# Optimization experiments

Hardware: AMD Instinct MI355X
Metric: run time of the kernel (lower is better)

The kernel has to match this reference:

```python
import jax, jax.numpy as jnp
import numpy as np

GROUP_SIZE = 64
IN_F, OUT_F, RANK = 4096, 4096, 32
N_TOKENS = 4096
N_GROUPS = IN_F // GROUP_SIZE


def setup_inputs() -> dict:
    key = jax.random.key(0)
    k = jax.random.split(key, 6)
    x = jax.random.normal(k[0], (N_TOKENS, IN_F), dtype=jnp.float32)
    # signed int4 values in [-8, 7], stored unpacked as int32
    main_qweight = jax.random.randint(k[1], (OUT_F, N_GROUPS, GROUP_SIZE), -8, 8, dtype=jnp.int32)
    main_wscale = jax.random.uniform(k[2], (OUT_F, N_GROUPS), dtype=jnp.float32) * 0.02 + 1e-3
    bias = jax.random.normal(k[3], (OUT_F,), dtype=jnp.float32) * 0.02
    proj_down_dense = jax.random.normal(k[4], (IN_F, RANK), dtype=jnp.float32) * 0.02
    proj_up_dense = jax.random.normal(k[5], (RANK, OUT_F), dtype=jnp.float32) * 0.02
    return {
        "x": x,
        "main_qweight": main_qweight,
        "main_wscale": main_wscale,
        "bias": bias,
        "proj_down_dense": proj_down_dense,
        "proj_up_dense": proj_up_dense,
    }


def reference(x, main_qweight, main_wscale, bias, proj_down_dense, proj_up_dense):
    n = x.shape[0]
    # --- per-group int8 activation quantization (symmetric, max-abs/127) ---
    xg = x.reshape(n, N_GROUPS, GROUP_SIZE).astype(jnp.float32)  # [N, G, gs]
    max_abs = jnp.max(jnp.abs(xg), axis=-1, keepdims=True)
    ascale = jnp.where(max_abs > 0, max_abs * (1.0 / 127.0), jnp.ones_like(max_abs))
    qx = jnp.clip(jnp.round(xg / ascale), -127.0, 127.0)
    # Fold per-group activation scales back in; per (out, group) weight scales into weight.
    # out[n,o] = sum_g ascale[n,g] * wscale[o,g] * sum_k qx[n,g,k] * qw[o,g,k]
    a_deq = (qx * ascale).reshape(n, IN_F)                                   # [N, in]
    w_deq = (main_qweight.astype(jnp.float32) * main_wscale[..., None]).reshape(OUT_F, IN_F)  # [out, in]
    out = a_deq @ w_deq.T + bias.astype(jnp.float32)                          # [N, out], fp32 accumulate
    # --- SVD low-rank correction: x @ proj_down @ proj_up (down in x dtype, up in fp32) ---
    low_rank = x @ proj_down_dense                                            # [N, rank]
    out = out + low_rank.astype(jnp.float32) @ proj_up_dense.astype(jnp.float32)
    return out.astype(x.dtype)
```

## Files before the change

### kernel.cpp

```cpp
#include <hip/hip_runtime.h>
#include <hip/hip_bf16.h>

#define IN_F  4096
#define OUT_F 4096
#define NTOK  4096
#define RANK  32
#define GS    64
#define NG    64
#define KTOT  4160
#define NKT   65
#define ITERS 32
#define KCH   1024

typedef __attribute__((ext_vector_type(4))) float f32x4;
typedef __attribute__((ext_vector_type(8))) short bf16x8;

#define AS1 __attribute__((address_space(1)))
#define AS3 __attribute__((address_space(3)))

__device__ __forceinline__ ushort f2bf(float f) {
  union { float f; uint u; } c; c.f = f;
  const uint u = c.u;
  return (ushort)((u + 0x7fffu + ((u >> 16) & 1u)) >> 16);
}

__global__ __launch_bounds__(256)
void prep_kernel(const float* __restrict__ x, const int* __restrict__ qw,
                 const float* __restrict__ wsc, const float* __restrict__ pd,
                 const float* __restrict__ pu, ushort* __restrict__ Aext,
                 ushort* __restrict__ Bext, ushort* __restrict__ pdT)
{
  const int bid = blockIdx.x;
  if (bid < 16384) {
    const int tid  = threadIdx.x;
    const int wave = tid >> 6, lane = tid & 63;
    const int sub  = lane & 15;
    const int ggrp = bid * 16 + wave * 4 + (lane >> 4);
    const int row  = ggrp >> 6, g = ggrp & 63;

    const float4 v = *(const float4*)(x + (size_t)row * IN_F + g * GS + sub * 4);
    float m = fmaxf(fmaxf(fabsf(v.x), fabsf(v.y)), fmaxf(fabsf(v.z), fabsf(v.w)));
    m = fmaxf(m, __shfl_xor(m, 1));
    m = fmaxf(m, __shfl_xor(m, 2));
    m = fmaxf(m, __shfl_xor(m, 4));
    m = fmaxf(m, __shfl_xor(m, 8));
    const float ascale = (m > 0.f) ? m * (1.f / 127.f) : 1.f;

    const float d0 = fminf(fmaxf(rintf(v.x / ascale), -127.f), 127.f) * ascale;
    const float d1 = fminf(fmaxf(rintf(v.y / ascale), -127.f), 127.f) * ascale;
    const float d2 = fminf(fmaxf(rintf(v.z / ascale), -127.f), 127.f) * ascale;
    const float d3 = fminf(fmaxf(rintf(v.w / ascale), -127.f), 127.f) * ascale;

    uint2 st;
    st.x = (uint)f2bf(d0) | ((uint)f2bf(d1) << 16);
    st.y = (uint)f2bf(d2) | ((uint)f2bf(d3) << 16);
    *(uint2*)(Aext + (size_t)row * KTOT + g * GS + sub * 4) = st;
  } else if (bid < 24576) {
    const int gidx = (bid - 16384) * 256 + threadIdx.x;
    const int o  = gidx >> 9;
    const int i0 = (gidx & 511) << 3;
    const float sc = wsc[o * NG + (i0 >> 6)];
    const int4 qa = *(const int4*)(qw + (size_t)o * IN_F + i0);
    const int4 qb = *(const int4*)(qw + (size_t)o * IN_F + i0 + 4);
    uint4 st;
    st.x = (uint)f2bf(qa.x * sc) | ((uint)f2bf(qa.y * sc) << 16);
    st.y = (uint)f2bf(qa.z * sc) | ((uint)f2bf(qa.w * sc) << 16);
    st.z = (uint)f2bf(qb.x * sc) | ((uint)f2bf(qb.y * sc) << 16);
    st.w = (uint)f2bf(qb.z * sc) | ((uint)f2bf(qb.w * sc) << 16);
    *(uint4*)(Bext + (size_t)o * KTOT + i0) = st;
  } else {
    const int id = (bid - 24576) * 256 + threadIdx.x;
    ushort* dst = Bext + (size_t)id * KTOT + IN_F;
    #pragma unroll
    for (int r = 0; r < RANK; ++r) {
      dst[r]        = f2bf(pu[(size_t)r * OUT_F + id]);
      dst[RANK + r] = 0;
    }
    #pragma unroll
    for (int r = 0; r < RANK; ++r)
      pdT[(size_t)r * IN_F + id] = f2bf(pd[(size_t)id * RANK + r]);
  }
}

__global__ __launch_bounds__(256)
void lr_kernel(const ushort* __restrict__ A, const ushort* __restrict__ pdT,
               float* __restrict__ part)
{
  __shared__ alignas(16) ushort lA[64 * 64];
  const int tid  = threadIdx.x;
  const int wave = tid >> 6, lane = tid & 63;
  const int mt = blockIdx.x >> 2;
  const int kc = blockIdx.x & 3;
  const int k0 = kc * KCH;

  const int tr  = tid >> 3;
  const int scc = (tid & 7) ^ (tr & 7);
  const ushort* aSrc = A + (size_t)(mt * 64 + tr) * KTOT + k0 + scc * 8;
  char* ldsA = (char*)lA + wave * 1024;

  f32x4 acc[2];
  #pragma unroll
  for (int n = 0; n < 2; ++n) acc[n] = f32x4{0.f, 0.f, 0.f, 0.f};

  for (int kt = 0; kt < KCH / 64; ++kt) {
    const ushort* aS = aSrc + kt * 64;
    #pragma unroll
    for (int j = 0; j < 2; ++j)
      __builtin_amdgcn_global_load_lds(
          (const AS1 void*)(aS + (size_t)j * 32 * KTOT),
          (AS3 void*)(ldsA + j * 4096), 16, 0, 0);
    __syncthreads();
    #pragma unroll
    for (int ks = 0; ks < 2; ++ks) {
      const int kb  = (ks * 32 + (lane >> 4) * 8) * 2;
      const int row = wave * 16 + (lane & 15);
      const int addr = (row * 128 + kb) ^ ((row & 7) << 4);
      bf16x8 af = *(const bf16x8*)((const char*)lA + addr);
      #pragma unroll
      for (int n = 0; n < 2; ++n) {
        const int prow = n * 16 + (lane & 15);
        bf16x8 bf = *(const bf16x8*)(pdT + (size_t)prow * IN_F + k0 + kt * 64 + ks * 32 + (lane >> 4) * 8);
        acc[n] = __builtin_amdgcn_mfma_f32_16x16x32_bf16(af, bf, acc[n], 0, 0, 0);
      }
    }
    __syncthreads();
  }
  const int r0   = lane & 15;
  const int rowb = mt * 64 + wave * 16 + (lane >> 4) * 4;
  #pragma unroll
  for (int n = 0; n < 2; ++n)
    #pragma unroll
    for (int i = 0; i < 4; ++i)
      part[((size_t)kc * 4096 + rowb + i) * 32 + n * 16 + r0] = acc[n][i];
}

__global__ __launch_bounds__(256)
void lrcomb_kernel(const float* __restrict__ part, ushort* __restrict__ Aext)
{
  const int id  = blockIdx.x * 256 + threadIdx.x;
  const int row = id >> 5, r = id & 31;
  const float s = part[(size_t)row * 32 + r]
                + part[(size_t)(4096 + row) * 32 + r]
                + part[(size_t)(8192 + row) * 32 + r]
                + part[(size_t)(12288 + row) * 32 + r];
  ushort* dst = Aext + (size_t)row * KTOT + IN_F;
  dst[r]        = f2bf(s);
  dst[RANK + r] = 0;
}

#define READ_AF8(DST, B_, MQ_)                                                   \
  { _Pragma("unroll")                                                            \
    for (int mf = 0; mf < 4; ++mf) {                                             \
      DST[mf][0] = *(const bf16x8*)(lds + afB0 + ((B_) * 32768 + (MQ_) * 8192 + mf * 2048)); \
      DST[mf][1] = *(const bf16x8*)(lds + afB1 + ((B_) * 32768 + (MQ_) * 8192 + mf * 2048)); \
    } }

#define READ_BF4(DST, B_, NQ_)                                                   \
  { _Pragma("unroll")                                                            \
    for (int nf = 0; nf < 2; ++nf) {                                             \
      DST[nf][0] = *(const bf16x8*)(lds + bfB0 + ((B_) * 32768 + (NQ_) * 4096 + nf * 2048)); \
      DST[nf][1] = *(const bf16x8*)(lds + bfB1 + ((B_) * 32768 + (NQ_) * 4096 + nf * 2048)); \
    } }

#define MFMA16(MQ_, NQ_, AF, BF)                                                 \
  _Pragma("unroll")                                                              \
  for (int mf = 0; mf < 4; ++mf)                                                 \
    _Pragma("unroll")                                                            \
    for (int nf = 0; nf < 2; ++nf)                                               \
      _Pragma("unroll")                                                          \
      for (int ks = 0; ks < 2; ++ks)                                             \
        acc[(MQ_) * 4 + mf][(NQ_) * 2 + nf] =                                    \
            __builtin_amdgcn_mfma_f32_16x16x32_bf16(AF[mf][ks], BF[nf][ks],      \
                acc[(MQ_) * 4 + mf][(NQ_) * 2 + nf], 0, 0, 0);

#define STAGE_A(B_, S0, S1, D0, D1, T_)                                          \
  { const ushort* s0 = Atile + S0 + (T_) * 64;                                   \
    const ushort* s1 = Atile + S1 + (T_) * 64;                                   \
    __builtin_amdgcn_global_load_lds((const AS1 void*)s0,                        \
        (AS3 void*)(lds + (B_) * 32768 + D0), 16, 0, 0);                         \
    __builtin_amdgcn_global_load_lds((const AS1 void*)s1,                        \
        (AS3 void*)(lds + (B_) * 32768 + D1), 16, 0, 0); }

#define STAGE_B(B_, S0, S1, D0, D1, T_)                                          \
  { const ushort* s0 = Btile + S0 + (T_) * 64;                                   \
    const ushort* s1 = Btile + S1 + (T_) * 64;                                   \
    __builtin_amdgcn_global_load_lds((const AS1 void*)s0,                        \
        (AS3 void*)(lds + 65536 + (B_) * 32768 + D0), 16, 0, 0);                 \
    __builtin_amdgcn_global_load_lds((const AS1 void*)s1,                        \
        (AS3 void*)(lds + 65536 + (B_) * 32768 + D1), 16, 0, 0); }

#define BAR __builtin_amdgcn_s_barrier()
#define DRAIN4 asm volatile("s_waitcnt vmcnt(4)" ::: "memory")
#define PRIO1 __builtin_amdgcn_s_setprio(1)
#define PRIO0 __builtin_amdgcn_s_setprio(0)

__global__ __launch_bounds__(512, 2)
void gemm256_kernel(const ushort* __restrict__ A, const ushort* __restrict__ B,
                    const float* __restrict__ bias, float* __restrict__ C)
{
  extern __shared__ char lds[];
  const int tid = threadIdx.x;
  const int w = tid >> 6, lane = tid & 63;
  const int l15 = lane & 15;
  const int wm = w >> 2, wn = w & 3;

  const int swz0 = (l15 * 128 + (lane >> 4) * 16) ^ ((l15 & 7) << 4);
  const int swz1 = (l15 * 128 + 64 + (lane >> 4) * 16) ^ ((l15 & 7) << 4);
  const int afB0 = wm * 16384 + swz0;
  const int afB1 = wm * 16384 + swz1;
  const int bfB0 = 65536 + wn * 8192 + swz0;
  const int bfB1 = 65536 + wn * 8192 + swz1;

  const int coff = ((lane & 7) ^ (lane >> 3)) << 3;
  const int g0 = w * 2, g1 = w * 2 + 1;
  const int aq0 = (g0 >> 3) * 2, asub0 = g0 & 7;
  const int aq1 = (g1 >> 3) * 2, asub1 = g1 & 7;
  const int aS00 = (aq0 * 64 + asub0 * 8 + (lane >> 3)) * KTOT + coff;
  const int aS01 = (aq1 * 64 + asub1 * 8 + (lane >> 3)) * KTOT + coff;
  const int aS10 = ((aq0 + 1) * 64 + asub0 * 8 + (lane >> 3)) * KTOT + coff;
  const int aS11 = ((aq1 + 1) * 64 + asub1 * 8 + (lane >> 3)) * KTOT + coff;
  const int aD00 = aq0 * 8192 + asub0 * 1024;
  const int aD01 = aq1 * 8192 + asub1 * 1024;
  const int aD10 = (aq0 + 1) * 8192 + asub0 * 1024;
  const int aD11 = (aq1 + 1) * 8192 + asub1 * 1024;
  const int bj0 = g0 >> 2, bsub0 = g0 & 3;
  const int bj1 = g1 >> 2, bsub1 = g1 & 3;
  const int bS00 = (bj0 * 64 + bsub0 * 8 + (lane >> 3)) * KTOT + coff;
  const int bS01 = (bj1 * 64 + bsub1 * 8 + (lane >> 3)) * KTOT + coff;
  const int bS10 = (bj0 * 64 + 32 + bsub0 * 8 + (lane >> 3)) * KTOT + coff;
  const int bS11 = (bj1 * 64 + 32 + bsub1 * 8 + (lane >> 3)) * KTOT + coff;
  const int bD00 = bj0 * 8192 + bsub0 * 1024;
  const int bD01 = bj1 * 8192 + bsub1 * 1024;
  const int bD10 = bj0 * 8192 + 4096 + bsub0 * 1024;
  const int bD11 = bj1 * 8192 + 4096 + bsub1 * 1024;

  const int xcd = blockIdx.x & 7, idx = blockIdx.x >> 3;
  const int bm = (xcd >> 1) * 4 + (idx >> 3);
  const int bn = (xcd & 1) * 8 + (idx & 7);

  const ushort* Atile = A + (size_t)bm * 256 * KTOT;
  const ushort* Btile = B + (size_t)bn * 256 * KTOT;

  f32x4 acc[8][4];
  #pragma unroll
  for (int m = 0; m < 8; ++m)
    #pragma unroll
    for (int n = 0; n < 4; ++n)
      acc[m][n] = f32x4{0.f, 0.f, 0.f, 0.f};

  bf16x8 afA[4][2], af2[4][2], b0[2][2], b1[2][2];

  STAGE_A(0, aS00, aS01, aD00, aD01, 0);
  STAGE_B(0, bS00, bS01, bD00, bD01, 0);
  STAGE_A(0, aS10, aS11, aD10, aD11, 0);
  STAGE_B(0, bS10, bS11, bD10, bD11, 0);
  STAGE_A(1, aS00, aS01, aD00, aD01, 1);
  STAGE_B(1, bS00, bS01, bD00, bD01, 1);
  DRAIN4;
  BAR;

  #pragma unroll 1
  for (int j = 0; j < ITERS; ++j) {
    const int t1 = 2 * j + 1;
    const int t2 = 2 * j + 2;
    const int t3 = (2 * j + 3 < NKT) ? 2 * j + 3 : NKT - 1;

    READ_AF8(afA, 0, 0);
    READ_BF4(b0, 0, 0);
    READ_BF4(b1, 0, 1);
    STAGE_A(1, aS10, aS11, aD10, aD11, t1);
    STAGE_B(1, bS10, bS11, bD10, bD11, t1);
    BAR;
    PRIO1; MFMA16(0, 0, afA, b0); MFMA16(0, 1, afA, b1); PRIO0;
    BAR;
    READ_AF8(af2, 0, 1);
    STAGE_A(0, aS00, aS01, aD00, aD01, t2);
    STAGE_B(0, bS00, bS01, bD00, bD01, t2);
    BAR;
    PRIO1; MFMA16(1, 0, af2, b0); MFMA16(1, 1, af2, b1); PRIO0;
    DRAIN4;
    BAR;
    READ_AF8(afA, 1, 0);
    READ_BF4(b0, 1, 0);
    READ_BF4(b1, 1, 1);
    STAGE_A(0, aS10, aS11, aD10, aD11, t2);
    STAGE_B(0, bS10, bS11, bD10, bD11, t2);
    BAR;
    PRIO1; MFMA16(0, 0, afA, b0); MFMA16(0, 1, afA, b1); PRIO0;
    BAR;
    READ_AF8(af2, 1, 1);
    STAGE_A(1, aS00, aS01, aD00, aD01, t3);
    STAGE_B(1, bS00, bS01, bD00, bD01, t3);
    BAR;
    PRIO1; MFMA16(1, 0, af2, b0); MFMA16(1, 1, af2, b1); PRIO0;
    DRAIN4;
    BAR;
  }

  READ_AF8(afA, 0, 0);
  READ_BF4(b0, 0, 0);
  READ_BF4(b1, 0, 1);
  MFMA16(0, 0, afA, b0); MFMA16(0, 1, afA, b1);
  READ_AF8(af2, 0, 1);
  MFMA16(1, 0, af2, b0); MFMA16(1, 1, af2, b1);

  const int csub = lane >> 4;
  #pragma unroll
  for (int nf = 0; nf < 4; ++nf) {
    const int col = bn * 256 + wn * 64 + nf * 16 + l15;
    const float bv = bias[col];
    #pragma unroll
    for (int mf = 0; mf < 8; ++mf) {
      const int row = bm * 256 + wm * 128 + mf * 16 + csub * 4;
      #pragma unroll
      for (int i = 0; i < 4; ++i)
        C[(size_t)(row + i) * OUT_F + col] = acc[mf][nf][i] + bv;
    }
  }
}

extern "C" void kernel_launch(void* const* d_in, const int* in_sizes, int n_in,
                              void* d_out, int out_size, void* d_ws, size_t ws_size,
                              hipStream_t stream) {
  const float* x    = (const float*)d_in[0];
  const int*   qw   = (const int*)d_in[1];
  const float* wsc  = (const float*)d_in[2];
  const float* bias = (const float*)d_in[3];
  const float* pd   = (const float*)d_in[4];
  const float* pu   = (const float*)d_in[5];
  float* out = (float*)d_out;

  ushort* Aext = (ushort*)d_ws;
  ushort* Bext = Aext + (size_t)NTOK * KTOT;
  ushort* pdT  = Bext + (size_t)OUT_F * KTOT;
  float*  part = (float*)(pdT + (size_t)RANK * IN_F);

  hipFuncSetAttribute(reinterpret_cast<const void*>(gemm256_kernel),
                      hipFuncAttributeMaxDynamicSharedMemorySize, 131072);

  prep_kernel  <<<24592, 256, 0, stream>>>(x, qw, wsc, pd, pu, Aext, Bext, pdT);
  lr_kernel    <<<  256, 256, 0, stream>>>(Aext, pdT, part);
  lrcomb_kernel<<<  512, 256, 0, stream>>>(part, Aext);
  gemm256_kernel<<< 256, 512, 131072, stream>>>(Aext, Bext, bias, out);
}
```

Baseline: 171.3 us.

## Split main loop into eight finer-grained phases with snake-ordered MFMA quadrants

Restructures the inner GEMM loop from four phases into eight. Each phase issues one quadrant of MFMAs and interleaves a single A or B staging load. The quadrants follow a snake order so A/B fragment registers are reused across adjacent phases, and only one fragment set is kept live. This aims to reduce register pressure and spread global-to-LDS traffic more evenly against compute, at the cost of twice as many barriers per iteration.

Measured after the change: 170.6 us. No clear change (-0.4%).

```diff
diff --git a/kernel.cpp b/kernel.cpp
--- a/kernel.cpp
+++ b/kernel.cpp
@@ -193,6 +193,17 @@
 #define DRAIN4 asm volatile("s_waitcnt vmcnt(4)" ::: "memory")
 #define PRIO1 __builtin_amdgcn_s_setprio(1)
 #define PRIO0 __builtin_amdgcn_s_setprio(0)
+
+#define PHASE(B_, MQ_, NQ_, READA, READB, BF_, STAGE, W4)                        \
+  {                                                                              \
+    if (READA) READ_AF8(af, B_, MQ_);                                            \
+    if (READB) READ_BF4(BF_, B_, NQ_);                                           \
+    STAGE;                                                                       \
+    BAR;                                                                         \
+    PRIO1; MFMA16(MQ_, NQ_, af, BF_); PRIO0;                                     \
+    if (W4) DRAIN4;                                                              \
+    BAR;                                                                         \
+  }
 
 __global__ __launch_bounds__(512, 2)
 void gemm256_kernel(const ushort* __restrict__ A, const ushort* __restrict__ B,
@@ -248,8 +259,6 @@
     for (int n = 0; n < 4; ++n)
       acc[m][n] = f32x4{0.f, 0.f, 0.f, 0.f};
 
-  bf16x8 afA[4][2], af2[4][2], b0[2][2], b1[2][2];
-
   STAGE_A(0, aS00, aS01, aD00, aD01, 0);
   STAGE_B(0, bS00, bS01, bD00, bD01, 0);
   STAGE_A(0, aS10, aS11, aD10, aD11, 0);
@@ -264,45 +273,26 @@
     const int t1 = 2 * j + 1;
     const int t2 = 2 * j + 2;
     const int t3 = (2 * j + 3 < NKT) ? 2 * j + 3 : NKT - 1;
-
-    READ_AF8(afA, 0, 0);
+    bf16x8 af[4][2], b0[2][2], b1[2][2];
+    PHASE(0, 0, 0, 1, 1, b0, { STAGE_B(1, bS10, bS11, bD10, bD11, t1); }, 0)
+    PHASE(0, 0, 1, 0, 1, b1, { STAGE_A(1, aS10, aS11, aD10, aD11, t1); }, 0)
+    PHASE(0, 1, 1, 1, 0, b1, { STAGE_A(0, aS00, aS01, aD00, aD01, t2); }, 0)
+    PHASE(0, 1, 0, 0, 0, b0, { STAGE_B(0, bS00, bS01, bD00, bD01, t2); }, 1)
+    PHASE(1, 0, 0, 1, 1, b0, { STAGE_B(0, bS10, bS11, bD10, bD11, t2); }, 0)
+    PHASE(1, 0, 1, 0, 1, b1, { STAGE_A(0, aS10, aS11, aD10, aD11, t2); }, 0)
+    PHASE(1, 1, 1, 1, 0, b1, { STAGE_A(1, aS00, aS01, aD00, aD01, t3); }, 0)
+    PHASE(1, 1, 0, 0, 0, b0, { STAGE_B(1, bS00, bS01, bD00, bD01, t3); }, 1)
+  }
+
+  {
+    bf16x8 af[4][2], b0[2][2], b1[2][2];
+    READ_AF8(af, 0, 0);
     READ_BF4(b0, 0, 0);
     READ_BF4(b1, 0, 1);
-    STAGE_A(1, aS10, aS11, aD10, aD11, t1);
-    STAGE_B(1, bS10, bS11, bD10, bD11, t1);
-    BAR;
-    PRIO1; MFMA16(0, 0, afA, b0); MFMA16(0, 1, afA, b1); PRIO0;
-    BAR;
-    READ_AF8(af2, 0, 1);
-    STAGE_A(0, aS00, aS01, aD00, aD01, t2);
-    STAGE_B(0, bS00, bS01, bD00, bD01, t2);
-    BAR;
-    PRIO1; MFMA16(1, 0, af2, b0); MFMA16(1, 1, af2, b1); PRIO0;
-    DRAIN4;
-    BAR;
-    READ_AF8(afA, 1, 0);
-    READ_BF4(b0, 1, 0);
-    READ_BF4(b1, 1, 1);
-    STAGE_A(0, aS10, aS11, aD10, aD11, t2);
-    STAGE_B(0, bS10, bS11, bD10, bD11, t2);
-    BAR;
-    PRIO1; MFMA16(0, 0, afA, b0); MFMA16(0, 1, afA, b1); PRIO0;
-    BAR;
-    READ_AF8(af2, 1, 1);
-    STAGE_A(1, aS00, aS01, aD00, aD01, t3);
-    STAGE_B(1, bS00, bS01, bD00, bD01, t3);
-    BAR;
-    PRIO1; MFMA16(1, 0, af2, b0); MFMA16(1, 1, af2, b1); PRIO0;
-    DRAIN4;
-    BAR;
-  }
-
-  READ_AF8(afA, 0, 0);
-  READ_BF4(b0, 0, 0);
-  READ_BF4(b1, 0, 1);
-  MFMA16(0, 0, afA, b0); MFMA16(0, 1, afA, b1);
-  READ_AF8(af2, 0, 1);
-  MFMA16(1, 0, af2, b0); MFMA16(1, 1, af2, b1);
+    MFMA16(0, 0, af, b0); MFMA16(0, 1, af, b1);
+    READ_AF8(af, 0, 1);
+    MFMA16(1, 0, af, b0); MFMA16(1, 1, af, b1);
+  }
 
   const int csub = lane >> 4;
   #pragma unroll
```
